# Optimization experiments

Hardware: AMD Instinct MI355X
Metric: run time of the kernel (lower is better)

## Reference

```python
import jax, jax.numpy as jnp
import numpy as np

B, XDIM, TWIN, INCH = 1024, 62, 10, 128
MID, OUT, K, K1, LIN, HC = 256, 512, 3, 10, 512, 4
EPS = 1e-5

REGIONS = [
    list(range(0, 5)),
    list(range(5, 8)) + list(range(14, 17)),
    list(range(8, 11)) + list(range(17, 20)),
    list(range(11, 14)) + list(range(20, 23)),
    list(range(23, 26)) + list(range(32, 35)),
    list(range(26, 29)) + list(range(35, 38)),
    list(range(29, 32)) + list(range(38, 41)),
    list(range(41, 44)) + list(range(50, 52)) + list(range(57, 58)),
    list(range(44, 47)) + list(range(52, 55)) + list(range(58, 61)),
    list(range(47, 50)) + list(range(55, 57)) + list(range(61, 62)),
]


def setup_inputs() -> dict:
    key = jax.random.key(0)
    ks = jax.random.split(key, 40)
    n = lambda k, s, sc=0.02: jax.random.normal(k, s, jnp.float32) * sc
    inp = {
        "x": jax.random.normal(ks[0], (B, XDIM, TWIN, INCH), jnp.float32),
        "tfe_w": n(ks[1], (XDIM, TWIN)),          # depthwise Conv2d (10,1) weight, squeezed
        "tfe_b": jnp.zeros((XDIM,), jnp.float32),
        "cheby1_w": n(ks[2], (K, INCH, OUT)),
        "A": n(ks[3], (XDIM, XDIM)),
        "cheby2_w": n(ks[4], (K, MID, OUT)),
        "A1": n(ks[5], (K1, K1)),
        "b_gate": jnp.float32(1.0),
        "c_gate": jnp.float32(1.0),
        "region_b": jnp.zeros((K1, MID), jnp.float32),
        "hc_w1": n(ks[6], (OUT * 72, LIN)),
        "hc_b1": jnp.zeros((LIN,), jnp.float32),
        "bn1_g": jnp.ones((LIN,), jnp.float32),
        "bn1_b": jnp.zeros((LIN,), jnp.float32),
        "hc_w2": n(ks[7], (LIN, LIN // 2)),
        "hc_b2": jnp.zeros((LIN // 2,), jnp.float32),
        "bn2_g": jnp.ones((LIN // 2,), jnp.float32),
        "bn2_b": jnp.zeros((LIN // 2,), jnp.float32),
        "hc_w3": n(ks[8], (LIN // 2, HC)),
        "hc_b3": jnp.zeros((HC,), jnp.float32),
    }
    for i, idx in enumerate(REGIONS):
        inp[f"rw{i+1}"] = n(ks[10 + i], (MID, INCH, len(idx)))
    return inp


def _cheby(x, L, Ws):
    # sum_k  S_k @ x @ W_k  with S_0 = I, S_k = S_{k-1} @ L ; then ReLU
    S = jnp.eye(L.shape[0], dtype=x.dtype)
    res = jnp.zeros(x.shape[:2] + (Ws.shape[-1],), x.dtype)
    for k in range(Ws.shape[0]):
        res = res + jnp.einsum("nm,bmt,to->bno", S, x, Ws[k])
        S = S @ L
    return jax.nn.relu(res)


def _bn(h, g, b):
    mu = h.mean(axis=0)
    v = h.var(axis=0)  # biased, training-mode BatchNorm1d
    return (h - mu) * jax.lax.rsqrt(v + EPS) * g + b


def _forward(x, tfe_w, tfe_b, cheby1_w, A, cheby2_w, A1, b_gate, c_gate,
             rw1, rw2, rw3, rw4, rw5, rw6, rw7, rw8, rw9, rw10, region_b,
             hc_w1, hc_b1, bn1_g, bn1_b, hc_w2, hc_b2, bn2_g, bn2_b, hc_w3, hc_b3):
    # variance gate (torch.var default: unbiased)
    sigma = jnp.var(x, axis=2, ddof=1)                              # (B, 62, INCH)
    g_tfe = jnp.einsum("bcit,ci->bct", x, tfe_w) + tfe_b[None, :, None]
    g = g_tfe * jnp.exp(-sigma)                                      # (B, 62, INCH)

    g1 = _cheby(g, A, cheby1_w)                                      # (B, 62, OUT)

    rws = [rw1, rw2, rw3, rw4, rw5, rw6, rw7, rw8, rw9, rw10]
    RG = []
    for i, (idx, w) in enumerate(zip(REGIONS, rws)):
        reg = g[:, jnp.asarray(idx), :]                              # (B, L, INCH)
        RG.append(jnp.einsum("blc,mcl->bm", reg, w) + region_b[i])   # Conv1d, full-width kernel
    g2in = jnp.stack(RG, axis=1)                                     # (B, 10, MID)
    g2 = _cheby(g2in, A1, cheby2_w)                                  # (B, 10, OUT)

    att = jnp.concatenate([b_gate * g1, c_gate * g2], axis=1)        # (B, 72, OUT)
    cat = jnp.concatenate([g1, g2], axis=1)
    out = jax.nn.softmax(att, axis=1) * cat
    out = out.reshape(out.shape[0], -1)                              # (B, 72*OUT)

    h = jax.nn.gelu(_bn(out @ hc_w1 + hc_b1, bn1_g, bn1_b), approximate=False)
    h = jax.nn.gelu(_bn(h @ hc_w2 + hc_b2, bn2_g, bn2_b), approximate=False)
    h = h @ hc_w3 + hc_b3
    return jax.nn.softmax(h, axis=1)


def reference(x, tfe_w, tfe_b, cheby1_w, A, cheby2_w, A1, b_gate, c_gate,
              rw1, rw2, rw3, rw4, rw5, rw6, rw7, rw8, rw9, rw10, region_b,
              hc_w1, hc_b1, bn1_g, bn1_b, hc_w2, hc_b2, bn2_g, bn2_b, hc_w3, hc_b3):
    return _forward(x, tfe_w, tfe_b, cheby1_w, A, cheby2_w, A1, b_gate, c_gate,
                    rw1, rw2, rw3, rw4, rw5, rw6, rw7, rw8, rw9, rw10, region_b,
                    hc_w1, hc_b1, bn1_g, bn1_b, hc_w2, hc_b2, bn2_g, bn2_b, hc_w3, hc_b3)
```

## Files before the change

kernel.cpp:

```cpp
#include <hip/hip_runtime.h>
#include <math.h>


__constant__ int cRegIdx[10][9] = {
  {0,1,2,3,4,0,0,0,0},
  {5,6,7,14,15,16,0,0,0},
  {8,9,10,17,18,19,0,0,0},
  {11,12,13,20,21,22,0,0,0},
  {23,24,25,32,33,34,0,0,0},
  {26,27,28,35,36,37,0,0,0},
  {29,30,31,38,39,40,0,0,0},
  {41,42,43,50,51,57,0,0,0},
  {44,45,46,52,53,54,58,59,60},
  {47,48,49,55,56,61,0,0,0}
};
__constant__ int cRegLen[10] = {5,6,6,6,6,6,6,6,9,6};

struct Ptr10 { const float* p[10]; };

typedef __attribute__((ext_vector_type(8))) short bf16x8;
typedef __attribute__((ext_vector_type(4))) float f32x4;

__device__ __forceinline__ float gelu_exact(float v){
  return 0.5f * v * (1.0f + erff(v * 0.70710678118654752f));
}
__device__ __forceinline__ unsigned short f2bf(float f){
  unsigned u = __float_as_uint(f);
  unsigned r = (u + 0x7fffu + ((u >> 16) & 1u)) >> 16;
  return (unsigned short)r;
}
__device__ __forceinline__ float bf2f(unsigned short u){
  return __uint_as_float(((unsigned)u) << 16);
}
__device__ __forceinline__ void load_lds16(const unsigned short* g, unsigned short* l){
  __builtin_amdgcn_global_load_lds(
      (const __attribute__((address_space(1))) void*)g,
      (__attribute__((address_space(3))) void*)l, 16, 0, 0);
}

#define MAC16(a4,b4) \
  acc[0][0]=fmaf(a4.x,b4.x,acc[0][0]); acc[0][1]=fmaf(a4.x,b4.y,acc[0][1]); \
  acc[0][2]=fmaf(a4.x,b4.z,acc[0][2]); acc[0][3]=fmaf(a4.x,b4.w,acc[0][3]); \
  acc[1][0]=fmaf(a4.y,b4.x,acc[1][0]); acc[1][1]=fmaf(a4.y,b4.y,acc[1][1]); \
  acc[1][2]=fmaf(a4.y,b4.z,acc[1][2]); acc[1][3]=fmaf(a4.y,b4.w,acc[1][3]); \
  acc[2][0]=fmaf(a4.z,b4.x,acc[2][0]); acc[2][1]=fmaf(a4.z,b4.y,acc[2][1]); \
  acc[2][2]=fmaf(a4.z,b4.z,acc[2][2]); acc[2][3]=fmaf(a4.z,b4.w,acc[2][3]); \
  acc[3][0]=fmaf(a4.w,b4.x,acc[3][0]); acc[3][1]=fmaf(a4.w,b4.y,acc[3][1]); \
  acc[3][2]=fmaf(a4.w,b4.z,acc[3][2]); acc[3][3]=fmaf(a4.w,b4.w,acc[3][3]);

template<bool RELU>
__global__ __launch_bounds__(256) void k_mfma(
    const unsigned short* __restrict__ A, long lda,
    const unsigned short* __restrict__ BT, long ldb,
    void* __restrict__ Cv, int ldc, int kPerZ, long cStrideZ){
  __shared__ unsigned short As[128*32];
  __shared__ unsigned short Bs[128*32];
  int tid = threadIdx.x;
  int wave = tid >> 6, lane = tid & 63;
  int m0 = blockIdx.x * 128, n0 = blockIdx.y * 128;
  int kStart = blockIdx.z * kPerZ;
  int waveM = wave >> 1, waveN = wave & 1;
  int lr = lane >> 2, ch = lane & 3;
  int quad = lane >> 4, mrow = lane & 15;
  int swe = ((quad ^ (mrow & 3)) << 3);

  int rA0 = wave*32 + lr;
  int rA1 = rA0 + 16;
  int ce  = ((ch ^ (rA0 & 3)) << 3);
  const unsigned short* gA0 = A  + (long)(m0 + rA0)*lda + kStart + ce;
  const unsigned short* gA1 = A  + (long)(m0 + rA1)*lda + kStart + ce;
  const unsigned short* gB0 = BT + (long)(n0 + rA0)*ldb + kStart + ce;
  const unsigned short* gB1 = BT + (long)(n0 + rA1)*ldb + kStart + ce;
  unsigned short* lA0 = &As[(wave*32)*32];
  unsigned short* lA1 = &As[(wave*32+16)*32];
  unsigned short* lB0 = &Bs[(wave*32)*32];
  unsigned short* lB1 = &Bs[(wave*32+16)*32];

  f32x4 acc[4][4] = {};
  int nIter = kPerZ >> 5;
  for (int it = 0; it < nIter; ++it){
    long ko = (long)it << 5;
    load_lds16(gA0 + ko, lA0);
    load_lds16(gA1 + ko, lA1);
    load_lds16(gB0 + ko, lB0);
    load_lds16(gB1 + ko, lB1);
    __syncthreads();
    bf16x8 af[4], bfr[4];
#pragma unroll
    for (int mi = 0; mi < 4; mi++)
      af[mi] = *(const bf16x8*)&As[(waveM*64 + mi*16 + mrow)*32 + swe];
#pragma unroll
    for (int ni = 0; ni < 4; ni++)
      bfr[ni] = *(const bf16x8*)&Bs[(waveN*64 + ni*16 + mrow)*32 + swe];
#pragma unroll
    for (int mi = 0; mi < 4; mi++)
#pragma unroll
      for (int ni = 0; ni < 4; ni++)
        acc[mi][ni] = __builtin_amdgcn_mfma_f32_16x16x32_bf16(
            af[mi], bfr[ni], acc[mi][ni], 0, 0, 0);
    __syncthreads();
  }
  if (RELU){
    unsigned short* C = (unsigned short*)Cv;
#pragma unroll
    for (int mi = 0; mi < 4; mi++)
#pragma unroll
      for (int ni = 0; ni < 4; ni++){
        int col = n0 + waveN*64 + ni*16 + mrow;
#pragma unroll
        for (int r = 0; r < 4; r++){
          int row = m0 + waveM*64 + mi*16 + quad*4 + r;
          C[(long)row*ldc + col] = f2bf(fmaxf(acc[mi][ni][r], 0.f));
        }
      }
  } else {
    float* C = (float*)Cv + (long)blockIdx.z * cStrideZ;
#pragma unroll
    for (int mi = 0; mi < 4; mi++)
#pragma unroll
      for (int ni = 0; ni < 4; ni++){
        int col = n0 + waveN*64 + ni*16 + mrow;
#pragma unroll
        for (int r = 0; r < 4; r++){
          int row = m0 + waveM*64 + mi*16 + quad*4 + r;
          C[(long)row*ldc + col] = acc[mi][ni][r];
        }
      }
  }
}
template __global__ void k_mfma<true>(const unsigned short*, long, const unsigned short*, long, void*, int, int, long);
template __global__ void k_mfma<false>(const unsigned short*, long, const unsigned short*, long, void*, int, int, long);

__global__ __launch_bounds__(256) void k_transpose_bf16(
    const float* __restrict__ src, unsigned short* __restrict__ dst, int R, int C){
  __shared__ float t[32][33];
  int c0 = blockIdx.x * 32, r0 = blockIdx.y * 32;
  int tx = threadIdx.x & 31, ty = threadIdx.x >> 5;
#pragma unroll
  for (int i = 0; i < 4; i++){
    int r = ty + i*8;
    t[r][tx] = src[(long)(r0+r)*C + c0 + tx];
  }
  __syncthreads();
#pragma unroll
  for (int i = 0; i < 4; i++){
    int cc = ty + i*8;
    dst[(long)(c0+cc)*R + r0 + tx] = f2bf(t[tx][cc]);
  }
}

__global__ __launch_bounds__(128) void k_g(
    const float* __restrict__ x, const float* __restrict__ tw,
    const float* __restrict__ tb, float* __restrict__ gt,
    unsigned short* __restrict__ xcat){
  int bid = blockIdx.x;
  int b = bid / 62, n = bid - b*62;
  int t = threadIdx.x;
  const float* xp = x + (long)bid * 1280 + t;
  float s = 0.f, s2 = 0.f, gv = 0.f;
#pragma unroll
  for (int i = 0; i < 10; i++){
    float v = xp[(long)i*128];
    s += v; s2 = fmaf(v, v, s2);
    gv = fmaf(v, tw[n*10 + i], gv);
  }
  float mean = s * 0.1f;
  float var  = (s2 - 10.f*mean*mean) * (1.f/9.f);
  float res  = (gv + tb[n]) * expf(-var);
  gt[(long)n*131072 + b*128 + t]  = res;
  xcat[(long)b*23808 + n*384 + t] = f2bf(res);
}

__global__ __launch_bounds__(256) void k_spread_gemm(
    const float* __restrict__ A62, const float* __restrict__ Gt,
    float* __restrict__ Agt, unsigned short* __restrict__ xcat, int slot){
  __shared__ float As[16][68];
  __shared__ float Bs[16][68];
  int tid = threadIdx.x;
  int n0 = blockIdx.x * 64;
  int ar = tid >> 2, ac = (tid & 3) << 2;
  int br = tid >> 4, bc = (tid & 15) << 2;
  int tx = tid & 15, ty = tid >> 4;
  float acc[4][4] = {};
  for (int kt = 0; kt < 62; kt += 16){
    float4 av;
    av.x = (ar < 62 && kt+ac+0 < 62) ? A62[ar*62 + kt+ac+0] : 0.f;
    av.y = (ar < 62 && kt+ac+1 < 62) ? A62[ar*62 + kt+ac+1] : 0.f;
    av.z = (ar < 62 && kt+ac+2 < 62) ? A62[ar*62 + kt+ac+2] : 0.f;
    av.w = (ar < 62 && kt+ac+3 < 62) ? A62[ar*62 + kt+ac+3] : 0.f;
    float4 bv = make_float4(0.f,0.f,0.f,0.f);
    int kr = kt + br;
    if (kr < 62) bv = *(const float4*)(Gt + (long)kr*131072 + n0 + bc);
    As[ac+0][ar]=av.x; As[ac+1][ar]=av.y; As[ac+2][ar]=av.z; As[ac+3][ar]=av.w;
    *(float4*)(&Bs[br][bc]) = bv;
    __syncthreads();
#pragma unroll
    for (int k = 0; k < 16; k++){
      float4 a4 = *(const float4*)(&As[k][ty<<2]);
      float4 b4 = *(const float4*)(&Bs[k][tx<<2]);
      MAC16(a4,b4)
    }
    __syncthreads();
  }
  int col = n0 + (tx<<2);
  int b = col >> 7, c = col & 127;
#pragma unroll
  for (int i = 0; i < 4; i++){
    int row = (ty<<2) + i;
    if (row >= 62) continue;
    if (Agt) *(float4*)(Agt + (long)row*131072 + col) =
        make_float4(acc[i][0], acc[i][1], acc[i][2], acc[i][3]);
    ushort4 u = make_ushort4(f2bf(acc[i][0]), f2bf(acc[i][1]),
                             f2bf(acc[i][2]), f2bf(acc[i][3]));
    *(ushort4*)(xcat + (long)b*23808 + row*384 + slot*128 + c) = u;
  }
}

__global__ __launch_bounds__(256) void k_gemm_region(
    const float* __restrict__ Gt, Ptr10 rws, const float* __restrict__ regb,
    float* __restrict__ g2in){
  __shared__ float As[16][68];
  __shared__ float Bs[16][68];
  int z = blockIdx.z;
  int L = cRegLen[z];
  int K = L << 7;
  const float* rw = rws.p[z];
  int tid = threadIdx.x;
  int m0 = blockIdx.x * 64;
  int n0 = blockIdx.y * 64;
  int ar = tid >> 2, ac = (tid & 3) << 2;
  int nn = tid & 63, kk0 = (tid >> 6) << 2;
  int tx = tid & 15, ty = tid >> 4;
  float acc[4][4] = {};
  for (int kt = 0; kt < K; kt += 16){
    int q = kt + ac;
    int node = cRegIdx[z][q >> 7];
    float4 av = *(const float4*)(Gt + (long)node*131072 + (m0+ar)*128 + (q & 127));
    As[ac+0][ar]=av.x; As[ac+1][ar]=av.y; As[ac+2][ar]=av.z; As[ac+3][ar]=av.w;
#pragma unroll
    for (int u = 0; u < 4; u++){
      int qq = kt + kk0 + u;
      Bs[kk0+u][nn] = rw[(long)(n0+nn)*K + (qq & 127)*L + (qq >> 7)];
    }
    __syncthreads();
#pragma unroll
    for (int k = 0; k < 16; k++){
      float4 a4 = *(const float4*)(&As[k][ty<<2]);
      float4 b4 = *(const float4*)(&Bs[k][tx<<2]);
      MAC16(a4,b4)
    }
    __syncthreads();
  }
  int col = n0 + (tx<<2);
  float4 rb = *(const float4*)(regb + z*256 + col);
#pragma unroll
  for (int i = 0; i < 4; i++){
    int row = m0 + (ty<<2) + i;
    float4 v = make_float4(acc[i][0]+rb.x, acc[i][1]+rb.y, acc[i][2]+rb.z, acc[i][3]+rb.w);
    *(float4*)(g2in + (long)row*2560 + z*256 + col) = v;
  }
}

__global__ __launch_bounds__(256) void k_x2cat(
    const float* __restrict__ g2in, const float* __restrict__ A1,
    unsigned short* __restrict__ X2){
  __shared__ float sg[2560];
  __shared__ float sA1[100];
  __shared__ float sA2[100];
  int b = blockIdx.x, tid = threadIdx.x;
  for (int i = tid; i < 2560; i += 256) sg[i] = g2in[(long)b*2560 + i];
  if (tid < 100) sA1[tid] = A1[tid];
  __syncthreads();
  if (tid < 100){
    int n = tid/10, m = tid - n*10;
    float a = 0.f;
#pragma unroll
    for (int t = 0; t < 10; t++) a = fmaf(sA1[n*10+t], sA1[t*10+m], a);
    sA2[tid] = a;
  }
  __syncthreads();
  for (int i = tid; i < 2560; i += 256){
    int n = i >> 8, t = i & 255;
    float v1 = 0.f, v2 = 0.f;
#pragma unroll
    for (int m = 0; m < 10; m++){
      float gv = sg[(m<<8) + t];
      v1 = fmaf(sA1[n*10+m], gv, v1);
      v2 = fmaf(sA2[n*10+m], gv, v2);
    }
    long base = (long)b*7680 + n*768;
    X2[base + t]       = f2bf(sg[i]);
    X2[base + 256 + t] = f2bf(v1);
    X2[base + 512 + t] = f2bf(v2);
  }
}

__global__ __launch_bounds__(128) void k_softcat(
    const unsigned short* __restrict__ g1, const unsigned short* __restrict__ g2,
    const float* __restrict__ bg_, const float* __restrict__ cg_,
    unsigned short* __restrict__ outb){
  __shared__ float sc[72][128];
  int b = blockIdx.x;
  int oq = blockIdx.y * 128;
  int tid = threadIdx.x;
  int o = oq + tid;
#pragma unroll
  for (int j = 0; j < 62; j++) sc[j][tid] = bf2f(g1[((long)b*62 + j)*512 + o]);
#pragma unroll
  for (int j = 0; j < 10; j++) sc[62+j][tid] = bf2f(g2[((long)b*10 + j)*512 + o]);
  __syncthreads();
  float bg = *bg_, cg = *cg_;
  float mx = -1e30f;
#pragma unroll
  for (int j = 0; j < 72; j++){
    float av = (j < 62 ? bg : cg) * sc[j][tid];
    mx = fmaxf(mx, av);
  }
  float sum = 0.f;
#pragma unroll
  for (int j = 0; j < 72; j++){
    float av = (j < 62 ? bg : cg) * sc[j][tid];
    sum += expf(av - mx);
  }
  float inv = 1.f / sum;
#pragma unroll
  for (int j = 0; j < 72; j++){
    float v = sc[j][tid];
    float av = (j < 62 ? bg : cg) * v;
    outb[(long)b*36864 + j*512 + o] = f2bf(expf(av - mx) * inv * v);
  }
}

__global__ __launch_bounds__(256) void k_reduce(
    const float* __restrict__ P, const float* __restrict__ bias,
    float* __restrict__ h1){
  int idx = blockIdx.x*256 + threadIdx.x;
  float v = bias[idx & 511];
#pragma unroll
  for (int s = 0; s < 16; s++) v += P[(long)s*524288 + idx];
  h1[idx] = v;
}

__global__ __launch_bounds__(256) void k_stats(
    const float* __restrict__ h, int N, float* __restrict__ mu,
    float* __restrict__ rs){
  int j = blockIdx.x;
  int tid = threadIdx.x;
  float s = 0.f, s2 = 0.f;
  for (int b = tid; b < 1024; b += 256){
    float v = h[(long)b*N + j];
    s += v; s2 = fmaf(v, v, s2);
  }
#pragma unroll
  for (int o = 32; o > 0; o >>= 1){
    s  += __shfl_down(s, o);
    s2 += __shfl_down(s2, o);
  }
  __shared__ float aa[4], bb[4];
  int w = tid >> 6;
  if ((tid & 63) == 0){ aa[w] = s; bb[w] = s2; }
  __syncthreads();
  if (tid == 0){
    s  = aa[0]+aa[1]+aa[2]+aa[3];
    s2 = bb[0]+bb[1]+bb[2]+bb[3];
    float m = s * (1.f/1024.f);
    float var = s2 * (1.f/1024.f) - m*m;
    mu[j] = m;
    rs[j] = rsqrtf(var + 1e-5f);
  }
}

__global__ __launch_bounds__(256) void k_gemm_h2(
    const float* __restrict__ A, const float* __restrict__ Bw,
    const float* __restrict__ mu, const float* __restrict__ rs,
    const float* __restrict__ gam, const float* __restrict__ bet,
    const float* __restrict__ bias, float* __restrict__ C){
  const int K = 512, N = 256;
  __shared__ float As[16][68];
  __shared__ float Bs[16][68];
  int tid = threadIdx.x;
  int m0 = blockIdx.x * 64, n0 = blockIdx.y * 64;
  int ar = tid >> 2, ac = (tid & 3) << 2;
  int br = tid >> 4, bc = (tid & 15) << 2;
  int tx = tid & 15, ty = tid >> 4;
  float acc[4][4] = {};
  const float* Ap = A + (long)(m0+ar)*K + ac;
  const float* Bp = Bw + (long)br*N + n0 + bc;
  for (int kt = 0; kt < K; kt += 16){
    float4 av = *(const float4*)(Ap + kt);
    int kc = kt + ac;
    av.x = gelu_exact((av.x - mu[kc+0])*rs[kc+0]*gam[kc+0] + bet[kc+0]);
    av.y = gelu_exact((av.y - mu[kc+1])*rs[kc+1]*gam[kc+1] + bet[kc+1]);
    av.z = gelu_exact((av.z - mu[kc+2])*rs[kc+2]*gam[kc+2] + bet[kc+2]);
    av.w = gelu_exact((av.w - mu[kc+3])*rs[kc+3]*gam[kc+3] + bet[kc+3]);
    float4 bv = *(const float4*)(Bp + (long)kt*N);
    As[ac+0][ar]=av.x; As[ac+1][ar]=av.y; As[ac+2][ar]=av.z; As[ac+3][ar]=av.w;
    *(float4*)(&Bs[br][bc]) = bv;
    __syncthreads();
#pragma unroll
    for (int k = 0; k < 16; k++){
      float4 a4 = *(const float4*)(&As[k][ty<<2]);
      float4 b4 = *(const float4*)(&Bs[k][tx<<2]);
      MAC16(a4,b4)
    }
    __syncthreads();
  }
  int col = n0 + (tx<<2);
  float4 bb = *(const float4*)(bias + col);
#pragma unroll
  for (int i = 0; i < 4; i++){
    float4 v = make_float4(acc[i][0]+bb.x, acc[i][1]+bb.y, acc[i][2]+bb.z, acc[i][3]+bb.w);
    *(float4*)(C + (long)(m0+(ty<<2)+i)*N + col) = v;
  }
}

__global__ __launch_bounds__(256) void k_final(
    const float* __restrict__ h2, const float* __restrict__ mu,
    const float* __restrict__ rs, const float* __restrict__ gam,
    const float* __restrict__ bet, const float* __restrict__ w3,
    const float* __restrict__ b3, float* __restrict__ outp){
  int b = blockIdx.x, tid = threadIdx.x;
  float v = h2[(long)b*256 + tid];
  v = (v - mu[tid]) * rs[tid] * gam[tid] + bet[tid];
  v = gelu_exact(v);
  float4 w = ((const float4*)w3)[tid];
  float p0 = v*w.x, p1 = v*w.y, p2 = v*w.z, p3 = v*w.w;
#pragma unroll
  for (int o = 32; o > 0; o >>= 1){
    p0 += __shfl_down(p0, o);
    p1 += __shfl_down(p1, o);
    p2 += __shfl_down(p2, o);
    p3 += __shfl_down(p3, o);
  }
  __shared__ float red[4][4];
  int wv = tid >> 6;
  if ((tid & 63) == 0){ red[wv][0]=p0; red[wv][1]=p1; red[wv][2]=p2; red[wv][3]=p3; }
  __syncthreads();
  if (tid == 0){
    float l[4];
#pragma unroll
    for (int c = 0; c < 4; c++)
      l[c] = red[0][c]+red[1][c]+red[2][c]+red[3][c] + b3[c];
    float m = fmaxf(fmaxf(l[0], l[1]), fmaxf(l[2], l[3]));
    float e[4]; float sum = 0.f;
#pragma unroll
    for (int c = 0; c < 4; c++){ e[c] = expf(l[c]-m); sum += e[c]; }
    float inv = 1.f / sum;
#pragma unroll
    for (int c = 0; c < 4; c++) outp[(long)b*4 + c] = e[c]*inv;
  }
}

extern "C" void kernel_launch(void* const* d_in, const int* in_sizes, int n_in,
                              void* d_out, int out_size, void* d_ws, size_t ws_size,
                              hipStream_t stream){
  (void)n_in; (void)out_size; (void)ws_size;
  bool dictOrder = (in_sizes[9] == 2560);
  const float* x     = (const float*)d_in[0];
  const float* tfe_w = (const float*)d_in[1];
  const float* tfe_b = (const float*)d_in[2];
  const float* ch1w  = (const float*)d_in[3];
  const float* Amat  = (const float*)d_in[4];
  const float* ch2w  = (const float*)d_in[5];
  const float* A1mat = (const float*)d_in[6];
  const float* bgate = (const float*)d_in[7];
  const float* cgate = (const float*)d_in[8];
  const float* regb  = (const float*)d_in[dictOrder ? 9 : 19];
  int o = dictOrder ? 0 : 10;
  const float* hc_w1 = (const float*)d_in[10+o];
  const float* hc_b1 = (const float*)d_in[11+o];
  const float* bn1g  = (const float*)d_in[12+o];
  const float* bn1b  = (const float*)d_in[13+o];
  const float* hc_w2 = (const float*)d_in[14+o];
  const float* hc_b2 = (const float*)d_in[15+o];
  const float* bn2g  = (const float*)d_in[16+o];
  const float* bn2b  = (const float*)d_in[17+o];
  const float* hc_w3 = (const float*)d_in[18+o];
  const float* hc_b3 = (const float*)d_in[19+o];
  Ptr10 rws;
  for (int i = 0; i < 10; i++) rws.p[i] = (const float*)d_in[(dictOrder ? 20 : 9) + i];

  char* Wb = (char*)d_ws;
  float*          GT    = (float*)(Wb + 0);
  unsigned short* XCAT  = (unsigned short*)(Wb + 32505856);
  float*          AGT   = (float*)(Wb + 81264640);
  float*          G2IN  = (float*)(Wb + 113770496);
  unsigned short* X2CAT = (unsigned short*)(Wb + 124256256);
  unsigned short* W1T   = (unsigned short*)(Wb + 139984896);
  unsigned short* WC1T  = (unsigned short*)(Wb + 177733632);
  unsigned short* WC2T  = (unsigned short*)(Wb + 178126848);
  unsigned short* G1    = (unsigned short*)(Wb + 178913280);
  unsigned short* G2    = (unsigned short*)(Wb + 243924992);
  unsigned short* OUTB  = (unsigned short*)(Wb + 0);
  float*          P     = (float*)(Wb + 81264640);
  float*          H1    = (float*)(Wb + 121634816);
  float*          H2    = (float*)(Wb + 123731968);
  float*          MU1   = (float*)(Wb + 124780544);
  float*          RS1   = MU1 + 512;
  float*          MU2   = MU1 + 1024;
  float*          RS2   = MU1 + 1280;

  k_transpose_bf16<<<dim3(16,1152), 256, 0, stream>>>(hc_w1, W1T, 36864, 512);
  k_transpose_bf16<<<dim3(16,12),   256, 0, stream>>>(ch1w,  WC1T, 384, 512);
  k_transpose_bf16<<<dim3(16,24),   256, 0, stream>>>(ch2w,  WC2T, 768, 512);

  k_g<<<1024*62, 128, 0, stream>>>(x, tfe_w, tfe_b, GT, XCAT);
  k_spread_gemm<<<2048, 256, 0, stream>>>(Amat, GT, AGT, XCAT, 1);
  k_spread_gemm<<<2048, 256, 0, stream>>>(Amat, AGT, nullptr, XCAT, 2);
  k_gemm_region<<<dim3(16,4,10), 256, 0, stream>>>(GT, rws, regb, G2IN);
  k_x2cat<<<1024, 256, 0, stream>>>(G2IN, A1mat, X2CAT);
  k_mfma<true><<<dim3(80,4,1), 256, 0, stream>>>(X2CAT, 768, WC2T, 768, (void*)G2, 512, 768, 0);
  k_mfma<true><<<dim3(496,4,1), 256, 0, stream>>>(XCAT, 384, WC1T, 384, (void*)G1, 512, 384, 0);
  k_softcat<<<dim3(1024,4), 128, 0, stream>>>(G1, G2, bgate, cgate, OUTB);
  k_mfma<false><<<dim3(8,4,16), 256, 0, stream>>>(OUTB, 36864, W1T, 36864, (void*)P, 512, 2304, 524288);
  k_reduce<<<2048, 256, 0, stream>>>(P, hc_b1, H1);
  k_stats<<<512, 256, 0, stream>>>(H1, 512, MU1, RS1);
  k_gemm_h2<<<dim3(16,4), 256, 0, stream>>>(H1, hc_w2, MU1, RS1, bn1g, bn1b, hc_b2, H2);
  k_stats<<<256, 256, 0, stream>>>(H2, 256, MU2, RS2);
  k_final<<<1024, 256, 0, stream>>>(H2, MU2, RS2, bn2g, bn2b, hc_w3, hc_b3, (float*)d_out);
}
```

Before: 1.012 ms.

## Replace fp32 spread and region GEMMs with precomputed A², per-batch spread, and MFMA region GEMM

Precomputes A and A² once (transposed) so both Chebyshev spread terms come from one per-batch kernel that holds the graph signal in LDS. This replaces two chained fp32 GEMMs and the fp32 AGT intermediate. The region GEMM now runs as a bf16 MFMA kernel over a region-ordered bf16 copy of G, with the region weights pre-transposed to bf16. The fp32 GT buffer is dropped and the workspace is re-laid out. In exchange, the A² path now reads bf16-rounded inputs, which adds precision risk, and the spread kernel uses a large per-thread register array.

```diff
diff --git a/kernel.cpp b/kernel.cpp
--- a/kernel.cpp
+++ b/kernel.cpp
@@ -2,19 +2,25 @@
 #include <math.h>
 
 
-__constant__ int cRegIdx[10][9] = {
-  {0,1,2,3,4,0,0,0,0},
-  {5,6,7,14,15,16,0,0,0},
-  {8,9,10,17,18,19,0,0,0},
-  {11,12,13,20,21,22,0,0,0},
-  {23,24,25,32,33,34,0,0,0},
-  {26,27,28,35,36,37,0,0,0},
-  {29,30,31,38,39,40,0,0,0},
-  {41,42,43,50,51,57,0,0,0},
-  {44,45,46,52,53,54,58,59,60},
-  {47,48,49,55,56,61,0,0,0}
+__constant__ int cOrder[62] = {
+  0,1,2,3,4,
+  5,6,7,14,15,16,
+  8,9,10,17,18,19,
+  11,12,13,20,21,22,
+  23,24,25,32,33,34,
+  26,27,28,35,36,37,
+  29,30,31,38,39,40,
+  41,42,43,50,51,57,
+  44,45,46,52,53,54,58,59,60,
+  47,48,49,55,56,61
 };
-__constant__ int cRegLen[10] = {5,6,6,6,6,6,6,6,9,6};
+__constant__ int cPos[62] = {
+  0,1,2,3,4, 5,6,7, 11,12,13, 17,18,19, 8,9,10, 14,15,16, 20,21,22,
+  23,24,25, 29,30,31, 35,36,37, 26,27,28, 32,33,34, 38,39,40,
+  41,42,43, 47,48,49, 56,57,58, 44,45, 50,51,52, 59,60, 46, 53,54,55, 61
+};
+__constant__ int cRegK[10]   = {640,768,768,768,768,768,768,768,1152,768};
+__constant__ int cRegCum[10] = {0,640,1408,2176,2944,3712,4480,5248,6016,7168};
 
 struct Ptr10 { const float* p[10]; };
 
@@ -131,6 +137,76 @@
 template __global__ void k_mfma<true>(const unsigned short*, long, const unsigned short*, long, void*, int, int, long);
 template __global__ void k_mfma<false>(const unsigned short*, long, const unsigned short*, long, void*, int, int, long);
 
+__global__ __launch_bounds__(256) void k_mfma_region(
+    const unsigned short* __restrict__ ARb,
+    const unsigned short* __restrict__ RWT,
+    const float* __restrict__ regb, float* __restrict__ g2in){
+  __shared__ unsigned short As[128*32];
+  __shared__ unsigned short Bs[128*32];
+  int z = blockIdx.z;
+  int K = cRegK[z];
+  int cumk = cRegCum[z];
+  const unsigned short* A  = ARb + cumk;
+  const unsigned short* BT = RWT + (long)cumk*256;
+  long lda = 7936, ldb = K;
+  int tid = threadIdx.x;
+  int wave = tid >> 6, lane = tid & 63;
+  int m0 = blockIdx.x * 128, n0 = blockIdx.y * 128;
+  int waveM = wave >> 1, waveN = wave & 1;
+  int lr = lane >> 2, ch = lane & 3;
+  int quad = lane >> 4, mrow = lane & 15;
+  int swe = ((quad ^ (mrow & 3)) << 3);
+
+  int rA0 = wave*32 + lr;
+  int rA1 = rA0 + 16;
+  int ce  = ((ch ^ (rA0 & 3)) << 3);
+  const unsigned short* gA0 = A  + (long)(m0 + rA0)*lda + ce;
+  const unsigned short* gA1 = A  + (long)(m0 + rA1)*lda + ce;
+  const unsigned short* gB0 = BT + (long)(n0 + rA0)*ldb + ce;
+  const unsigned short* gB1 = BT + (long)(n0 + rA1)*ldb + ce;
+  unsigned short* lA0 = &As[(wave*32)*32];
+  unsigned short* lA1 = &As[(wave*32+16)*32];
+  unsigned short* lB0 = &Bs[(wave*32)*32];
+  unsigned short* lB1 = &Bs[(wave*32+16)*32];
+
+  f32x4 acc[4][4] = {};
+  int nIter = K >> 5;
+  for (int it = 0; it < nIter; ++it){
+    long ko = (long)it << 5;
+    load_lds16(gA0 + ko, lA0);
+    load_lds16(gA1 + ko, lA1);
+    load_lds16(gB0 + ko, lB0);
+    load_lds16(gB1 + ko, lB1);
+    __syncthreads();
+    bf16x8 af[4], bfr[4];
+#pragma unroll
+    for (int mi = 0; mi < 4; mi++)
+      af[mi] = *(const bf16x8*)&As[(waveM*64 + mi*16 + mrow)*32 + swe];
+#pragma unroll
+    for (int ni = 0; ni < 4; ni++)
+      bfr[ni] = *(const bf16x8*)&Bs[(waveN*64 + ni*16 + mrow)*32 + swe];
+#pragma unroll
+    for (int mi = 0; mi < 4; mi++)
+#pragma unroll
+      for (int ni = 0; ni < 4; ni++)
+        acc[mi][ni] = __builtin_amdgcn_mfma_f32_16x16x32_bf16(
+            af[mi], bfr[ni], acc[mi][ni], 0, 0, 0);
+    __syncthreads();
+  }
+#pragma unroll
+  for (int mi = 0; mi < 4; mi++)
+#pragma unroll
+    for (int ni = 0; ni < 4; ni++){
+      int col = n0 + waveN*64 + ni*16 + mrow;
+      float bias = regb[z*256 + col];
+#pragma unroll
+      for (int r = 0; r < 4; r++){
+        int row = m0 + waveM*64 + mi*16 + quad*4 + r;
+        g2in[(long)row*2560 + z*256 + col] = acc[mi][ni][r] + bias;
+      }
+    }
+}
+
 __global__ __launch_bounds__(256) void k_transpose_bf16(
     const float* __restrict__ src, unsigned short* __restrict__ dst, int R, int C){
   __shared__ float t[32][33];
@@ -149,9 +225,32 @@
   }
 }
 
+__global__ __launch_bounds__(128) void k_rwt(Ptr10 rws, unsigned short* __restrict__ RWT){
+  int z = blockIdx.y, m = blockIdx.x;
+  int K = cRegK[z], L = K >> 7;
+  const float* rw = rws.p[z] + (long)m*K;
+  unsigned short* dst = RWT + (long)cRegCum[z]*256 + (long)m*K;
+  for (int k = threadIdx.x; k < K; k += 128){
+    int l = k >> 7, c = k & 127;
+    dst[k] = f2bf(rw[c*L + l]);
+  }
+}
+
+__global__ __launch_bounds__(256) void k_a2(
+    const float* __restrict__ A, float* __restrict__ AT, float* __restrict__ A2T){
+  int tid = threadIdx.x;
+  for (int i = tid; i < 3844; i += 256){
+    int r = i / 62, cc = i - r*62;
+    AT[cc*62 + r] = A[r*62 + cc];
+    float s = 0.f;
+    for (int t = 0; t < 62; t++) s = fmaf(A[r*62 + t], A[t*62 + cc], s);
+    A2T[cc*62 + r] = s;
+  }
+}
+
 __global__ __launch_bounds__(128) void k_g(
     const float* __restrict__ x, const float* __restrict__ tw,
-    const float* __restrict__ tb, float* __restrict__ gt,
+    const float* __restrict__ tb, unsigned short* __restrict__ arb,
     unsigned short* __restrict__ xcat){
   int bid = blockIdx.x;
   int b = bid / 62, n = bid - b*62;
@@ -167,98 +266,35 @@
   float mean = s * 0.1f;
   float var  = (s2 - 10.f*mean*mean) * (1.f/9.f);
   float res  = (gv + tb[n]) * expf(-var);
-  gt[(long)n*131072 + b*128 + t]  = res;
-  xcat[(long)b*23808 + n*384 + t] = f2bf(res);
-}
-
-__global__ __launch_bounds__(256) void k_spread_gemm(
-    const float* __restrict__ A62, const float* __restrict__ Gt,
-    float* __restrict__ Agt, unsigned short* __restrict__ xcat, int slot){
-  __shared__ float As[16][68];
-  __shared__ float Bs[16][68];
-  int tid = threadIdx.x;
-  int n0 = blockIdx.x * 64;
-  int ar = tid >> 2, ac = (tid & 3) << 2;
-  int br = tid >> 4, bc = (tid & 15) << 2;
-  int tx = tid & 15, ty = tid >> 4;
-  float acc[4][4] = {};
-  for (int kt = 0; kt < 62; kt += 16){
-    float4 av;
-    av.x = (ar < 62 && kt+ac+0 < 62) ? A62[ar*62 + kt+ac+0] : 0.f;
-    av.y = (ar < 62 && kt+ac+1 < 62) ? A62[ar*62 + kt+ac+1] : 0.f;
-    av.z = (ar < 62 && kt+ac+2 < 62) ? A62[ar*62 + kt+ac+2] : 0.f;
-    av.w = (ar < 62 && kt+ac+3 < 62) ? A62[ar*62 + kt+ac+3] : 0.f;
-    float4 bv = make_float4(0.f,0.f,0.f,0.f);
-    int kr = kt + br;
-    if (kr < 62) bv = *(const float4*)(Gt + (long)kr*131072 + n0 + bc);
-    As[ac+0][ar]=av.x; As[ac+1][ar]=av.y; As[ac+2][ar]=av.z; As[ac+3][ar]=av.w;
-    *(float4*)(&Bs[br][bc]) = bv;
-    __syncthreads();
-#pragma unroll
-    for (int k = 0; k < 16; k++){
-      float4 a4 = *(const float4*)(&As[k][ty<<2]);
-      float4 b4 = *(const float4*)(&Bs[k][tx<<2]);
-      MAC16(a4,b4)
-    }
-    __syncthreads();
-  }
-  int col = n0 + (tx<<2);
-  int b = col >> 7, c = col & 127;
-#pragma unroll
-  for (int i = 0; i < 4; i++){
-    int row = (ty<<2) + i;
-    if (row >= 62) continue;
-    if (Agt) *(float4*)(Agt + (long)row*131072 + col) =
-        make_float4(acc[i][0], acc[i][1], acc[i][2], acc[i][3]);
-    ushort4 u = make_ushort4(f2bf(acc[i][0]), f2bf(acc[i][1]),
-                             f2bf(acc[i][2]), f2bf(acc[i][3]));
-    *(ushort4*)(xcat + (long)b*23808 + row*384 + slot*128 + c) = u;
-  }
-}
-
-__global__ __launch_bounds__(256) void k_gemm_region(
-    const float* __restrict__ Gt, Ptr10 rws, const float* __restrict__ regb,
-    float* __restrict__ g2in){
-  __shared__ float As[16][68];
-  __shared__ float Bs[16][68];
-  int z = blockIdx.z;
-  int L = cRegLen[z];
-  int K = L << 7;
-  const float* rw = rws.p[z];
-  int tid = threadIdx.x;
-  int m0 = blockIdx.x * 64;
-  int n0 = blockIdx.y * 64;
-  int ar = tid >> 2, ac = (tid & 3) << 2;
-  int nn = tid & 63, kk0 = (tid >> 6) << 2;
-  int tx = tid & 15, ty = tid >> 4;
-  float acc[4][4] = {};
-  for (int kt = 0; kt < K; kt += 16){
-    int q = kt + ac;
-    int node = cRegIdx[z][q >> 7];
-    float4 av = *(const float4*)(Gt + (long)node*131072 + (m0+ar)*128 + (q & 127));
-    As[ac+0][ar]=av.x; As[ac+1][ar]=av.y; As[ac+2][ar]=av.z; As[ac+3][ar]=av.w;
-#pragma unroll
-    for (int u = 0; u < 4; u++){
-      int qq = kt + kk0 + u;
-      Bs[kk0+u][nn] = rw[(long)(n0+nn)*K + (qq & 127)*L + (qq >> 7)];
-    }
-    __syncthreads();
-#pragma unroll
-    for (int k = 0; k < 16; k++){
-      float4 a4 = *(const float4*)(&As[k][ty<<2]);
-      float4 b4 = *(const float4*)(&Bs[k][tx<<2]);
-      MAC16(a4,b4)
-    }
-    __syncthreads();
-  }
-  int col = n0 + (tx<<2);
-  float4 rb = *(const float4*)(regb + z*256 + col);
-#pragma unroll
-  for (int i = 0; i < 4; i++){
-    int row = m0 + (ty<<2) + i;
-    float4 v = make_float4(acc[i][0]+rb.x, acc[i][1]+rb.y, acc[i][2]+rb.z, acc[i][3]+rb.w);
-    *(float4*)(g2in + (long)row*2560 + z*256 + col) = v;
-  }
+  unsigned short rb = f2bf(res);
+  arb[(long)b*7936 + cPos[n]*128 + t] = rb;
+  xcat[(long)b*23808 + n*384 + t]     = rb;
+}
+
+__global__ __launch_bounds__(256) void k_spread2(
+    const unsigned short* __restrict__ ARb, const float* __restrict__ AT,
+    const float* __restrict__ A2T, unsigned short* __restrict__ xcat){
+  __shared__ float sgn[7936];
+  int b = blockIdx.x, tid = threadIdx.x;
+  for (int i = tid; i < 7936; i += 256){
+    int p = i >> 7, c = i & 127;
+    sgn[cOrder[p]*128 + c] = bf2f(ARb[(long)b*7936 + i]);
+  }
+  __syncthreads();
+  int c = tid & 127, mat = tid >> 7;
+  const float* MT = mat ? A2T : AT;
+  float acc[62];
+#pragma unroll
+  for (int n = 0; n < 62; n++) acc[n] = 0.f;
+  for (int m = 0; m < 62; m++){
+    float gv = sgn[m*128 + c];
+    const float* Mp = MT + m*62;
+#pragma unroll
+    for (int n = 0; n < 62; n++) acc[n] = fmaf(Mp[n], gv, acc[n]);
+  }
+  long base = (long)b*23808 + (mat+1)*128 + c;
+#pragma unroll
+  for (int n = 0; n < 62; n++) xcat[base + (long)n*384] = f2bf(acc[n]);
 }
 
 __global__ __launch_bounds__(256) void k_x2cat(
@@ -481,33 +517,36 @@
   for (int i = 0; i < 10; i++) rws.p[i] = (const float*)d_in[(dictOrder ? 20 : 9) + i];
 
   char* Wb = (char*)d_ws;
-  float*          GT    = (float*)(Wb + 0);
-  unsigned short* XCAT  = (unsigned short*)(Wb + 32505856);
-  float*          AGT   = (float*)(Wb + 81264640);
-  float*          G2IN  = (float*)(Wb + 113770496);
-  unsigned short* X2CAT = (unsigned short*)(Wb + 124256256);
-  unsigned short* W1T   = (unsigned short*)(Wb + 139984896);
-  unsigned short* WC1T  = (unsigned short*)(Wb + 177733632);
-  unsigned short* WC2T  = (unsigned short*)(Wb + 178126848);
-  unsigned short* G1    = (unsigned short*)(Wb + 178913280);
-  unsigned short* G2    = (unsigned short*)(Wb + 243924992);
+  unsigned short* ARb   = (unsigned short*)(Wb + 0);
+  unsigned short* XCAT  = (unsigned short*)(Wb + 16252928);
+  unsigned short* RWT   = (unsigned short*)(Wb + 65011712);
+  float*          G2IN  = (float*)(Wb + 69074944);
+  unsigned short* X2CAT = (unsigned short*)(Wb + 79560704);
+  unsigned short* W1T   = (unsigned short*)(Wb + 95289344);
+  unsigned short* WC1T  = (unsigned short*)(Wb + 133038080);
+  unsigned short* WC2T  = (unsigned short*)(Wb + 133431296);
+  unsigned short* G1    = (unsigned short*)(Wb + 134217728);
+  unsigned short* G2    = (unsigned short*)(Wb + 199229440);
   unsigned short* OUTB  = (unsigned short*)(Wb + 0);
-  float*          P     = (float*)(Wb + 81264640);
-  float*          H1    = (float*)(Wb + 121634816);
-  float*          H2    = (float*)(Wb + 123731968);
-  float*          MU1   = (float*)(Wb + 124780544);
+  float*          P     = (float*)(Wb + 209715200);
+  float*          H1    = (float*)(Wb + 243269632);
+  float*          H2    = (float*)(Wb + 245366784);
+  float*          MU1   = (float*)(Wb + 246415360);
   float*          RS1   = MU1 + 512;
   float*          MU2   = MU1 + 1024;
   float*          RS2   = MU1 + 1280;
+  float*          AT    = (float*)(Wb + 246423552);
+  float*          A2T   = (float*)(Wb + 246439040);
 
   k_transpose_bf16<<<dim3(16,1152), 256, 0, stream>>>(hc_w1, W1T, 36864, 512);
   k_transpose_bf16<<<dim3(16,12),   256, 0, stream>>>(ch1w,  WC1T, 384, 512);
   k_transpose_bf16<<<dim3(16,24),   256, 0, stream>>>(ch2w,  WC2T, 768, 512);
-
-  k_g<<<1024*62, 128, 0, stream>>>(x, tfe_w, tfe_b, GT, XCAT);
-  k_spread_gemm<<<2048, 256, 0, stream>>>(Amat, GT, AGT, XCAT, 1);
-  k_spread_gemm<<<2048, 256, 0, stream>>>(Amat, AGT, nullptr, XCAT, 2);
-  k_gemm_region<<<dim3(16,4,10), 256, 0, stream>>>(GT, rws, regb, G2IN);
+  k_rwt<<<dim3(256,10), 128, 0, stream>>>(rws, RWT);
+  k_a2<<<1, 256, 0, stream>>>(Amat, AT, A2T);
+
+  k_g<<<1024*62, 128, 0, stream>>>(x, tfe_w, tfe_b, ARb, XCAT);
+  k_spread2<<<1024, 256, 0, stream>>>(ARb, AT, A2T, XCAT);
+  k_mfma_region<<<dim3(8,2,10), 256, 0, stream>>>(ARb, RWT, regb, G2IN);
   k_x2cat<<<1024, 256, 0, stream>>>(G2IN, A1mat, X2CAT);
   k_mfma<true><<<dim3(80,4,1), 256, 0, stream>>>(X2CAT, 768, WC2T, 768, (void*)G2, 512, 768, 0);
   k_mfma<true><<<dim3(496,4,1), 256, 0, stream>>>(XCAT, 384, WC1T, 384, (void*)G1, 512, 384, 0);
```

New measurement: 1.054 ms. 1.04x slower.
